# Kernel tuning notes

Hardware: AMD Instinct MI355X
Metric: run time of the kernel (lower is better)

The kernel has to match this reference:

```python
import jax, jax.numpy as jnp
import numpy as np

LN_EPS = 1e-5


def setup_inputs() -> dict:
    key = jax.random.key(0)
    kA, kX, kh = jax.random.split(key, 3)
    B, N, Cin, C, K = 16, 1024, 64, 64, 3
    A = jax.random.normal(kA, (B, N, N), dtype=jnp.float32)
    X = jax.random.normal(kX, (B, N, Cin), dtype=jnp.float32)
    h = jax.random.normal(kh, (K + 1, C, N), dtype=jnp.float32)
    ln_gamma = jnp.ones((C,), dtype=jnp.float32)
    ln_beta = jnp.zeros((C,), dtype=jnp.float32)
    return {"A": A, "X": X, "h": h, "ln_gamma": ln_gamma, "ln_beta": ln_beta}


def reference(A, X, h, ln_gamma, ln_beta):
    # Original loops compute, for each output channel c:
    #   sum_i sum_ch diag(h[i,c]) @ A^i @ X[..., ch]
    # which equals sum_i h[i,c,:] * (A^i @ X.sum(-1)).
    num_terms = h.shape[0] - 1  # static
    Xs = X.sum(-1)  # [B, N]
    powers = [Xs]
    p = Xs
    for _ in range(num_terms):  # static small loop over polynomial terms
        p = jnp.einsum('bnm,bm->bn', A, p)  # A^i @ Xs, matrix-vector per batch
        powers.append(p)
    P = jnp.stack(powers)  # [K+1, B, N]
    # node-variant per-channel taps: Y[b,n,c] = sum_i h[i,c,n] * P[i,b,n]
    Y = jnp.einsum('icn,ibn->bnc', h, P)  # [B, N, C]
    mu = Y.mean(axis=-1, keepdims=True)
    var = Y.var(axis=-1, keepdims=True)
    Yn = (Y - mu) / jnp.sqrt(var + LN_EPS) * ln_gamma + ln_beta
    return jnp.tanh(Yn)
```

## Files before the change

kernel.cpp:

```cpp
#include <hip/hip_runtime.h>
#include <math.h>

constexpr int B = 16, N = 1024, Cin = 64, C = 64, K = 3;
constexpr int BN = B * N;
constexpr int GRID = 512;
constexpr int ROWS = 32;
#define LN_EPS 1e-5f

__device__ __forceinline__ void bbar(unsigned int* cnt) {
    __syncthreads();
    if (threadIdx.x == 0) {
        __hip_atomic_fetch_add(cnt, 1u, __ATOMIC_RELAXED, __HIP_MEMORY_SCOPE_AGENT);
        int spins = 0;
        while (__hip_atomic_load(cnt, __ATOMIC_RELAXED, __HIP_MEMORY_SCOPE_AGENT) < 32u) {
            __builtin_amdgcn_s_sleep(8);
            if (++spins > (1 << 17)) break;
        }
    }
    __syncthreads();
}

__global__ void __launch_bounds__(256, 2)
fused_persist(const float* __restrict__ A, const float* __restrict__ X,
              const float* __restrict__ h, const float* __restrict__ gamma,
              const float* __restrict__ beta, float* __restrict__ out,
              unsigned int* __restrict__ bar, float* __restrict__ P) {
    __shared__ float hl[K + 1][ROWS][C];
    __shared__ __align__(16) float4 xs[N / 4];
    __shared__ float p3s[ROWS];
    const int tid   = threadIdx.x;
    const int lane  = tid & 63;
    const int w     = tid >> 6;
    const int b     = blockIdx.x >> 5;
    const int rbase = (blockIdx.x & 31) * ROWS;
    unsigned int* mybar = bar + (size_t)b * 3 * 32;

    const float* Ab = A + ((size_t)b << 20);
    float4 Ar[2][4][4];
    #pragma unroll
    for (int r = 0; r < 2; ++r)
        #pragma unroll
        for (int j = 0; j < 4; ++j) {
            const float4* rp = (const float4*)(Ab + (size_t)(rbase + r * 16 + w * 4 + j) * N);
            #pragma unroll
            for (int k = 0; k < 4; ++k)
                Ar[r][j][k] = rp[k * 64 + lane];
        }

    {
        const float* Xb = X + ((size_t)b * N + rbase) * Cin;
        float* P0 = P + (size_t)b * N;
        #pragma unroll
        for (int j = 0; j < 8; ++j) {
            int nn = w * 8 + j;
            float v = Xb[(size_t)nn * Cin + lane];
            #pragma unroll
            for (int off = 32; off; off >>= 1) v += __shfl_xor(v, off);
            if (lane == 0)
                __hip_atomic_store(&P0[rbase + nn], v, __ATOMIC_RELAXED,
                                   __HIP_MEMORY_SCOPE_AGENT);
        }
    }

    {
        const float* src = h + ((size_t)w * C + lane) * N + rbase;
        #pragma unroll
        for (int j4 = 0; j4 < 8; ++j4) {
            float4 v = ((const float4*)src)[j4];
            hl[w][j4 * 4 + 0][lane] = v.x;
            hl[w][j4 * 4 + 1][lane] = v.y;
            hl[w][j4 * 4 + 2][lane] = v.z;
            hl[w][j4 * 4 + 3][lane] = v.w;
        }
    }
    bbar(mybar);

    for (int it = 0; it < 3; ++it) {
        const float* xsrc = P + (size_t)it * BN + (size_t)b * N;
        xs[tid] = ((const float4*)xsrc)[tid];
        __syncthreads();

        float acc[2][4] = {{0.f, 0.f, 0.f, 0.f}, {0.f, 0.f, 0.f, 0.f}};
        #pragma unroll
        for (int k = 0; k < 4; ++k) {
            float4 xx = xs[k * 64 + lane];
            #pragma unroll
            for (int r = 0; r < 2; ++r)
                #pragma unroll
                for (int j = 0; j < 4; ++j) {
                    float4 a = Ar[r][j][k];
                    acc[r][j] += a.x * xx.x + a.y * xx.y + a.z * xx.z + a.w * xx.w;
                }
        }
        #pragma unroll
        for (int off = 32; off; off >>= 1)
            #pragma unroll
            for (int r = 0; r < 2; ++r)
                #pragma unroll
                for (int j = 0; j < 4; ++j)
                    acc[r][j] += __shfl_xor(acc[r][j], off);

        if (lane == 0) {
            if (it < 2) {
                float* ydst = P + (size_t)(it + 1) * BN + (size_t)b * N;
                #pragma unroll
                for (int r = 0; r < 2; ++r)
                    #pragma unroll
                    for (int j = 0; j < 4; ++j)
                        __hip_atomic_store(&ydst[rbase + r * 16 + w * 4 + j], acc[r][j],
                                           __ATOMIC_RELAXED, __HIP_MEMORY_SCOPE_AGENT);
            } else {
                #pragma unroll
                for (int r = 0; r < 2; ++r)
                    #pragma unroll
                    for (int j = 0; j < 4; ++j)
                        p3s[r * 16 + w * 4 + j] = acc[r][j];
            }
        }
        if (it < 2) bbar(mybar + (1 + it) * 32);
        else        __syncthreads();
    }

    const float g  = gamma[lane];
    const float be = beta[lane];
    #pragma unroll
    for (int j = 0; j < 8; ++j) {
        const int nn = w * 8 + j;
        const int n  = rbase + nn;
        float y = p3s[nn] * hl[3][nn][lane];
        #pragma unroll
        for (int i = 0; i < 3; ++i) {
            float pv = P[(size_t)i * BN + (size_t)b * N + n];
            y += pv * hl[i][nn][lane];
        }
        float s = y;
        #pragma unroll
        for (int off = 32; off; off >>= 1) s += __shfl_xor(s, off);
        float mu = s * (1.0f / 64.0f);
        float d  = y - mu;
        float v  = d * d;
        #pragma unroll
        for (int off = 32; off; off >>= 1) v += __shfl_xor(v, off);
        float var = v * (1.0f / 64.0f);
        float yn  = d * rsqrtf(var + LN_EPS) * g + be;
        out[((size_t)b * N + n) * C + lane] = tanhf(yn);
    }
}

extern "C" void kernel_launch(void* const* d_in, const int* in_sizes, int n_in,
                              void* d_out, int out_size, void* d_ws, size_t ws_size,
                              hipStream_t stream) {
    const float* A     = (const float*)d_in[0];
    const float* X     = (const float*)d_in[1];
    const float* h     = (const float*)d_in[2];
    const float* gamma = (const float*)d_in[3];
    const float* beta  = (const float*)d_in[4];
    float* out = (float*)d_out;

    unsigned int* bar = (unsigned int*)d_ws;
    float* P = (float*)((char*)d_ws + 8192);

    hipMemsetAsync(bar, 0, B * 3 * 32 * sizeof(unsigned int), stream);
    fused_persist<<<GRID, 256, 0, stream>>>(A, X, h, gamma, beta, out, bar, P);
}
```

Before: 123.3 us.

## Split resident A rows between registers and LDS, defer h staging to epilogue

Half of each block's 32 rows of A now stay in registers and the other 16 rows are staged in a 64KB LDS buffer. That buffer is unioned with the h tap table, which is now loaded only after the last matvec iteration, with a padded stride of 65 to avoid bank conflicts. The aim is to cut VGPR pressure from 128 float4 registers to 64, avoiding spills under the 2-blocks-per-CU launch bound. The cost is LDS reads inside every iteration and more shared memory per block, which at 64KB+ could limit co-residency needed by the persistent grid barrier.

```diff
diff --git a/kernel.cpp b/kernel.cpp
--- a/kernel.cpp
+++ b/kernel.cpp
@@ -25,7 +25,10 @@
               const float* __restrict__ h, const float* __restrict__ gamma,
               const float* __restrict__ beta, float* __restrict__ out,
               unsigned int* __restrict__ bar, float* __restrict__ P) {
-    __shared__ float hl[K + 1][ROWS][C];
+    __shared__ __align__(16) union SU {
+        float As[16][1024];
+        float hl[K + 1][ROWS][65];
+    } u;
     __shared__ __align__(16) float4 xs[N / 4];
     __shared__ float p3s[ROWS];
     const int tid   = threadIdx.x;
@@ -34,18 +37,31 @@
     const int b     = blockIdx.x >> 5;
     const int rbase = (blockIdx.x & 31) * ROWS;
     unsigned int* mybar = bar + (size_t)b * 3 * 32;
+    const float* Ab = A + ((size_t)b << 20);
 
-    const float* Ab = A + ((size_t)b << 20);
-    float4 Ar[2][4][4];
+    float4 Ar[4][4];
     #pragma unroll
-    for (int r = 0; r < 2; ++r)
+    for (int j = 0; j < 4; ++j) {
+        const float4* rp = (const float4*)(Ab + (size_t)(rbase + 16 + w * 4 + j) * N);
         #pragma unroll
-        for (int j = 0; j < 4; ++j) {
-            const float4* rp = (const float4*)(Ab + (size_t)(rbase + r * 16 + w * 4 + j) * N);
-            #pragma unroll
-            for (int k = 0; k < 4; ++k)
-                Ar[r][j][k] = rp[k * 64 + lane];
-        }
+        for (int k = 0; k < 4; ++k)
+            Ar[j][k] = rp[k * 64 + lane];
+    }
+    #pragma unroll
+    for (int j = 0; j < 4; ++j)
+        #pragma unroll
+        for (int k = 0; k < 4; ++k)
+            asm volatile("" : "+v"(Ar[j][k].x), "+v"(Ar[j][k].y),
+                              "+v"(Ar[j][k].z), "+v"(Ar[j][k].w));
+
+    #pragma unroll
+    for (int i = 0; i < 16; ++i) {
+        int idx  = i * 256 + tid;
+        int row  = idx >> 8;
+        int col4 = idx & 255;
+        ((float4*)u.As[row])[col4] =
+            ((const float4*)(Ab + (size_t)(rbase + row) * N))[col4];
+    }
 
     {
         const float* Xb = X + ((size_t)b * N + rbase) * Cin;
@@ -61,18 +77,6 @@
                                    __HIP_MEMORY_SCOPE_AGENT);
         }
     }
-
-    {
-        const float* src = h + ((size_t)w * C + lane) * N + rbase;
-        #pragma unroll
-        for (int j4 = 0; j4 < 8; ++j4) {
-            float4 v = ((const float4*)src)[j4];
-            hl[w][j4 * 4 + 0][lane] = v.x;
-            hl[w][j4 * 4 + 1][lane] = v.y;
-            hl[w][j4 * 4 + 2][lane] = v.z;
-            hl[w][j4 * 4 + 3][lane] = v.w;
-        }
-    }
     bbar(mybar);
 
     for (int it = 0; it < 3; ++it) {
@@ -80,46 +84,65 @@
         xs[tid] = ((const float4*)xsrc)[tid];
         __syncthreads();
 
-        float acc[2][4] = {{0.f, 0.f, 0.f, 0.f}, {0.f, 0.f, 0.f, 0.f}};
+        float accL[4] = {0.f, 0.f, 0.f, 0.f};
+        float accR[4] = {0.f, 0.f, 0.f, 0.f};
         #pragma unroll
         for (int k = 0; k < 4; ++k) {
             float4 xx = xs[k * 64 + lane];
             #pragma unroll
-            for (int r = 0; r < 2; ++r)
-                #pragma unroll
-                for (int j = 0; j < 4; ++j) {
-                    float4 a = Ar[r][j][k];
-                    acc[r][j] += a.x * xx.x + a.y * xx.y + a.z * xx.z + a.w * xx.w;
-                }
+            for (int j = 0; j < 4; ++j) {
+                float4 aL = ((const float4*)u.As[w * 4 + j])[k * 64 + lane];
+                accL[j] += aL.x * xx.x + aL.y * xx.y + aL.z * xx.z + aL.w * xx.w;
+                float4 aR = Ar[j][k];
+                accR[j] += aR.x * xx.x + aR.y * xx.y + aR.z * xx.z + aR.w * xx.w;
+            }
         }
         #pragma unroll
         for (int off = 32; off; off >>= 1)
             #pragma unroll
-            for (int r = 0; r < 2; ++r)
-                #pragma unroll
-                for (int j = 0; j < 4; ++j)
-                    acc[r][j] += __shfl_xor(acc[r][j], off);
+            for (int j = 0; j < 4; ++j) {
+                accL[j] += __shfl_xor(accL[j], off);
+                accR[j] += __shfl_xor(accR[j], off);
+            }
 
         if (lane == 0) {
             if (it < 2) {
-                float* ydst = P + (size_t)(it + 1) * BN + (size_t)b * N;
+                float* ydst = P + (size_t)(it + 1) * BN + (size_t)b * N + rbase;
                 #pragma unroll
-                for (int r = 0; r < 2; ++r)
-                    #pragma unroll
-                    for (int j = 0; j < 4; ++j)
-                        __hip_atomic_store(&ydst[rbase + r * 16 + w * 4 + j], acc[r][j],
-                                           __ATOMIC_RELAXED, __HIP_MEMORY_SCOPE_AGENT);
+                for (int j = 0; j < 4; ++j) {
+                    __hip_atomic_store(&ydst[w * 4 + j],      accL[j],
+                                       __ATOMIC_RELAXED, __HIP_MEMORY_SCOPE_AGENT);
+                    __hip_atomic_store(&ydst[16 + w * 4 + j], accR[j],
+                                       __ATOMIC_RELAXED, __HIP_MEMORY_SCOPE_AGENT);
+                }
             } else {
                 #pragma unroll
-                for (int r = 0; r < 2; ++r)
-                    #pragma unroll
-                    for (int j = 0; j < 4; ++j)
-                        p3s[r * 16 + w * 4 + j] = acc[r][j];
+                for (int j = 0; j < 4; ++j) {
+                    p3s[w * 4 + j]      = accL[j];
+                    p3s[16 + w * 4 + j] = accR[j];
+                }
             }
         }
         if (it < 2) bbar(mybar + (1 + it) * 32);
         else        __syncthreads();
     }
+
+    {
+        const int i4    = tid >> 6;
+        const int cofs  = (tid & 63) >> 3;
+        const int nngrp = tid & 7;
+        #pragma unroll
+        for (int c0 = 0; c0 < 64; c0 += 8) {
+            int c = c0 + cofs;
+            float4 v = *(const float4*)(h + ((size_t)i4 * C + c) * N + rbase + nngrp * 4);
+            int nn0 = nngrp * 4;
+            u.hl[i4][nn0 + 0][c] = v.x;
+            u.hl[i4][nn0 + 1][c] = v.y;
+            u.hl[i4][nn0 + 2][c] = v.z;
+            u.hl[i4][nn0 + 3][c] = v.w;
+        }
+    }
+    __syncthreads();
 
     const float g  = gamma[lane];
     const float be = beta[lane];
@@ -127,11 +150,11 @@
     for (int j = 0; j < 8; ++j) {
         const int nn = w * 8 + j;
         const int n  = rbase + nn;
-        float y = p3s[nn] * hl[3][nn][lane];
+        float y = p3s[nn] * u.hl[3][nn][lane];
         #pragma unroll
         for (int i = 0; i < 3; ++i) {
             float pv = P[(size_t)i * BN + (size_t)b * N + n];
-            y += pv * hl[i][nn][lane];
+            y += pv * u.hl[i][nn][lane];
         }
         float s = y;
         #pragma unroll
```

After: 121.0 us. No clear change (-1.9%).
